# Kernel optimization log

Measured on AMD Instinct MI355X. Metric: run time of the kernel, lower is better.

## Reference

```python
import jax, jax.numpy as jnp
import numpy as np

B, S, V, H, T = 128, 512, 600, 512, 121  # batch, enc steps, vocab, hidden, dec steps (batch_max_length+1)


def setup_inputs() -> dict:
    key = jax.random.key(0)
    ks = jax.random.split(key, 12)
    sc = lambda *shape: 1.0 / np.sqrt(shape[-1])
    inp = {
        "batch_H": jax.random.normal(ks[0], (B, S, V), dtype=jnp.float32),
        "text": jax.random.randint(ks[1], (B, T), 0, V, dtype=jnp.int64),
        # AttentionCell params
        "W_i2h": jax.random.normal(ks[2], (H, V), dtype=jnp.float32) * sc(H, V),
        "W_h2h": jax.random.normal(ks[3], (H, H), dtype=jnp.float32) * sc(H, H),
        "b_h2h": jnp.zeros((H,), dtype=jnp.float32),
        "W_score": jax.random.normal(ks[4], (1, H), dtype=jnp.float32) * sc(1, H),
        # LSTMCell params (torch gate order i, f, g, o); input = context(V) + onehot(V)
        "W_ih": jax.random.normal(ks[5], (4 * H, 2 * V), dtype=jnp.float32) * sc(4 * H, 2 * V),
        "W_hh": jax.random.normal(ks[6], (4 * H, H), dtype=jnp.float32) * sc(4 * H, H),
        "b_ih": jnp.zeros((4 * H,), dtype=jnp.float32),
        "b_hh": jnp.zeros((4 * H,), dtype=jnp.float32),
        # generator
        "W_gen": jax.random.normal(ks[7], (V, H), dtype=jnp.float32) * sc(V, H),
        "b_gen": jnp.zeros((V,), dtype=jnp.float32),
    }
    return inp


def reference(batch_H, text, W_i2h, W_h2h, b_h2h, W_score, W_ih, W_hh, b_ih, b_hh, W_gen, b_gen):
    # Training-path forward: teacher forcing over T = batch_max_length+1 steps.
    # text gets a GO (=0) column prepended; step i consumes text_pad[:, i].
    text_pad = jnp.concatenate([jnp.zeros((B, 1), dtype=text.dtype), text], axis=1)[:, :T]
    onehots = jax.nn.one_hot(text_pad, V, dtype=batch_H.dtype)  # [B, T, V]

    # i2h(batch_H) is constant across timesteps -> hoist out of the loop.
    H_proj = jnp.einsum("bsv,hv->bsh", batch_H, W_i2h)  # [B, S, H]

    def step(carry, onehot_t):
        h, c = carry
        prev_proj = h @ W_h2h.T + b_h2h  # [B, H]
        e = jnp.tanh(H_proj + prev_proj[:, None, :]) @ W_score[0]  # [B, S]
        alpha = jax.nn.softmax(e, axis=1)
        context = jnp.einsum("bs,bsv->bv", alpha, batch_H)  # [B, V]
        x = jnp.concatenate([context, onehot_t], axis=1)  # [B, 2V]
        gates = x @ W_ih.T + b_ih + h @ W_hh.T + b_hh  # [B, 4H]
        i_g, f_g, g_g, o_g = jnp.split(gates, 4, axis=1)
        c_new = jax.nn.sigmoid(f_g) * c + jax.nn.sigmoid(i_g) * jnp.tanh(g_g)
        h_new = jax.nn.sigmoid(o_g) * jnp.tanh(c_new)
        return (h_new, c_new), h_new

    h0 = jnp.zeros((B, H), dtype=batch_H.dtype)
    c0 = jnp.zeros((B, H), dtype=batch_H.dtype)
    _, hiddens = jax.lax.scan(step, (h0, c0), jnp.swapaxes(onehots, 0, 1))  # [T, B, H]
    output_hiddens = jnp.swapaxes(hiddens, 0, 1)  # [B, T, H]
    probs = jax.nn.softmax(output_hiddens @ W_gen.T + b_gen, axis=2)  # [B, T, V]
    return probs
```

## Files before the change

kernel.cpp:

```cpp
#include <hip/hip_runtime.h>
#include <hip/hip_fp16.h>
#include <stdint.h>

#define Bsz 128
#define Ssz 512
#define Vsz 600
#define Hsz 512
#define Tsz 121

__device__ __forceinline__ float fast_tanh(float x) {
  float e = __expf(x + x);
  return 1.0f - __fdividef(2.0f, 1.0f + e);
}

__global__ __launch_bounds__(256) void k_wt(const float* __restrict__ Wi,
                                            float* __restrict__ WiT) {
  __shared__ float T[32][25];
  int k0 = blockIdx.x * 24, c0 = blockIdx.y * 32;
  for (int idx = threadIdx.x; idx < 32 * 24; idx += 256) {
    int i = idx / 24, j = idx - i * 24;
    T[i][j] = Wi[(size_t)(c0 + i) * 600 + k0 + j];
  }
  __syncthreads();
  for (int idx = threadIdx.x; idx < 24 * 32; idx += 256) {
    int j = idx >> 5, i = idx & 31;
    WiT[(size_t)(k0 + j) * 512 + c0 + i] = T[i][j];
  }
}

__global__ __launch_bounds__(256) void k_hp(const float* __restrict__ bH,
                                            const float* __restrict__ WiT,
                                            __half* __restrict__ Hp,
                                            __half* __restrict__ bHT) {
  __shared__ __align__(16) float As[16][604];
  int m0 = blockIdx.x * 16;
  for (int idx = threadIdx.x; idx < 16 * 600; idx += 256) {
    int r = idx / 600, k = idx - r * 600;
    As[r][k] = bH[(size_t)(m0 + r) * 600 + k];
  }
  __syncthreads();
  {
    int b = blockIdx.x >> 5, s0 = (blockIdx.x & 31) * 16;
    for (int v = threadIdx.x; v < 600; v += 256) {
      __half hbuf[16];
#pragma unroll
      for (int r = 0; r < 16; ++r) hbuf[r] = __float2half(As[r][v]);
      float4* dst = (float4*)&bHT[((size_t)b * 600 + v) * 512 + s0];
      dst[0] = ((float4*)hbuf)[0];
      dst[1] = ((float4*)hbuf)[1];
    }
  }
  int rg = threadIdx.x & 3, cg = threadIdx.x >> 2;
  int r0 = rg * 4;
  for (int pass = 0; pass < 2; ++pass) {
    int c0 = pass * 256 + cg * 4;
    float acc[4][4] = {};
    for (int k = 0; k < 600; k += 4) {
      float4 w0 = *(const float4*)&WiT[(size_t)(k + 0) * 512 + c0];
      float4 w1 = *(const float4*)&WiT[(size_t)(k + 1) * 512 + c0];
      float4 w2 = *(const float4*)&WiT[(size_t)(k + 2) * 512 + c0];
      float4 w3 = *(const float4*)&WiT[(size_t)(k + 3) * 512 + c0];
#pragma unroll
      for (int i = 0; i < 4; ++i) {
        float4 a = *(const float4*)&As[r0 + i][k];
        acc[i][0] += a.x * w0.x + a.y * w1.x + a.z * w2.x + a.w * w3.x;
        acc[i][1] += a.x * w0.y + a.y * w1.y + a.z * w2.y + a.w * w3.y;
        acc[i][2] += a.x * w0.z + a.y * w1.z + a.z * w2.z + a.w * w3.z;
        acc[i][3] += a.x * w0.w + a.y * w1.w + a.z * w2.w + a.w * w3.w;
      }
    }
#pragma unroll
    for (int i = 0; i < 4; ++i) {
      __half2 p01 = __floats2half2_rn(acc[i][0], acc[i][1]);
      __half2 p23 = __floats2half2_rn(acc[i][2], acc[i][3]);
      union { __half2 h2[2]; float2 f2; } u;
      u.h2[0] = p01; u.h2[1] = p23;
      *(float2*)&Hp[(size_t)(m0 + r0 + i) * Hsz + c0] = u.f2;
    }
  }
}

__global__ __launch_bounds__(256) void k_pp(const float* __restrict__ hprev,
                                            const float* __restrict__ W,
                                            const float* __restrict__ bias,
                                            float* __restrict__ pp) {
  __shared__ __align__(16) float hs[512];
  __shared__ float part[128];
  int b = blockIdx.x, jq = blockIdx.y;
  int tid = threadIdx.x;
  hs[tid] = hprev[b * Hsz + tid];
  hs[tid + 256] = hprev[b * Hsz + 256 + tid];
  __syncthreads();
  int jl = tid & 127, kh = tid >> 7;
  int j = jq * 128 + jl;
  const float* wrow = W + (size_t)j * Hsz + kh * 256;
  const float* hp = hs + kh * 256;
  float acc = 0.f;
#pragma unroll 4
  for (int k = 0; k < 256; k += 4) {
    float4 w = *(const float4*)(wrow + k);
    float4 h4 = *(const float4*)(hp + k);
    acc += w.x * h4.x + w.y * h4.y + w.z * h4.z + w.w * h4.w;
  }
  if (kh == 1) part[jl] = acc;
  __syncthreads();
  if (kh == 0) pp[b * Hsz + j] = acc + part[jl] + bias[j];
}

__global__ __launch_bounds__(512) void k_e(const __half* __restrict__ Hp,
                                           const float* __restrict__ pp,
                                           const float* __restrict__ Wsc,
                                           float* __restrict__ ev) {
  __shared__ __align__(16) float pps[512];
  __shared__ __align__(16) float wss[512];
  __shared__ float part[4][128];
  int b = blockIdx.x >> 2, tile = blockIdx.x & 3;
  int tid = threadIdx.x;
  pps[tid] = pp[b * Hsz + tid];
  wss[tid] = Wsc[tid];
  __syncthreads();
  int sl = tid & 127, kq = tid >> 7;
  int s = tile * 128 + sl;
  const __half* hrow = Hp + ((size_t)b * Ssz + s) * Hsz + kq * 128;
  const float* pk = pps + kq * 128;
  const float* wk = wss + kq * 128;
  float acc = 0.f;
#pragma unroll 8
  for (int k = 0; k < 128; k += 8) {
    float4 raw = *(const float4*)(hrow + k);
    const __half2* h2p = (const __half2*)&raw;
    float2 f0 = __half22float2(h2p[0]);
    float2 f1 = __half22float2(h2p[1]);
    float2 f2 = __half22float2(h2p[2]);
    float2 f3 = __half22float2(h2p[3]);
    acc += wk[k + 0] * fast_tanh(f0.x + pk[k + 0]);
    acc += wk[k + 1] * fast_tanh(f0.y + pk[k + 1]);
    acc += wk[k + 2] * fast_tanh(f1.x + pk[k + 2]);
    acc += wk[k + 3] * fast_tanh(f1.y + pk[k + 3]);
    acc += wk[k + 4] * fast_tanh(f2.x + pk[k + 4]);
    acc += wk[k + 5] * fast_tanh(f2.y + pk[k + 5]);
    acc += wk[k + 6] * fast_tanh(f3.x + pk[k + 6]);
    acc += wk[k + 7] * fast_tanh(f3.y + pk[k + 7]);
  }
  part[kq][sl] = acc;
  __syncthreads();
  if (kq == 0)
    ev[b * Ssz + s] = (part[0][sl] + part[1][sl]) + (part[2][sl] + part[3][sl]);
}

__global__ __launch_bounds__(256) void k_ctx(const __half* __restrict__ bHT,
                                             const float* __restrict__ ev,
                                             float* __restrict__ ctx) {
  __shared__ __align__(16) float al[512];
  __shared__ float red[8];
  int b = blockIdx.x, vc = blockIdx.y;
  int tid = threadIdx.x, wv = tid >> 6, ln = tid & 63;
  float e0 = ev[b * Ssz + tid], e1 = ev[b * Ssz + 256 + tid];
  float m = fmaxf(e0, e1);
#pragma unroll
  for (int off = 32; off > 0; off >>= 1) m = fmaxf(m, __shfl_xor(m, off));
  if (ln == 0) red[wv] = m;
  __syncthreads();
  m = fmaxf(fmaxf(red[0], red[1]), fmaxf(red[2], red[3]));
  float x0 = __expf(e0 - m), x1 = __expf(e1 - m);
  float sum = x0 + x1;
#pragma unroll
  for (int off = 32; off > 0; off >>= 1) sum += __shfl_xor(sum, off);
  if (ln == 0) red[4 + wv] = sum;
  __syncthreads();
  sum = (red[4] + red[5]) + (red[6] + red[7]);
  float inv = __fdividef(1.f, sum);
  al[tid] = x0 * inv;
  al[tid + 256] = x1 * inv;
  __syncthreads();
  int v = vc * 200 + tid;
  if (tid < 200) {
    const __half* row = bHT + ((size_t)b * Vsz + v) * Ssz;
    float a0 = 0.f, a1 = 0.f, a2 = 0.f, a3 = 0.f;
#pragma unroll 8
    for (int s = 0; s < Ssz; s += 8) {
      float4 raw = *(const float4*)(row + s);
      const __half2* h2p = (const __half2*)&raw;
      float2 f0 = __half22float2(h2p[0]);
      float2 f1 = __half22float2(h2p[1]);
      float2 f2 = __half22float2(h2p[2]);
      float2 f3 = __half22float2(h2p[3]);
      float4 aa = *(const float4*)&al[s];
      float4 ab = *(const float4*)&al[s + 4];
      a0 += aa.x * f0.x + aa.y * f0.y;
      a1 += aa.z * f1.x + aa.w * f1.y;
      a2 += ab.x * f2.x + ab.y * f2.y;
      a3 += ab.z * f3.x + ab.w * f3.y;
    }
    ctx[b * Vsz + v] = (a0 + a1) + (a2 + a3);
  }
}

struct ShG { float xs[8][1112]; float4 part[8][32]; };

__global__ __launch_bounds__(512) void k_gates(
    const float* __restrict__ ctx, const float* __restrict__ hprev,
    const float* __restrict__ Wih, const float* __restrict__ Whh,
    const float* __restrict__ bih, const float* __restrict__ bhh,
    const int* __restrict__ text, int t,
    const float* __restrict__ cin, float* __restrict__ cout,
    float* __restrict__ hnextf, __half* __restrict__ hnext16) {
  __shared__ __align__(16) ShG G;
  const int bid = blockIdx.x, tid = threadIdx.x;
  const int jt = (bid & 7) * 2 + ((bid >> 3) & 1);
  const int bt = bid >> 4;
  int b0 = bt * 8, j0 = jt * 32;
  for (int idx = tid; idx < 8 * 600; idx += 512) {
    int r = idx / 600, k = idx - r * 600;
    G.xs[r][k] = ctx[(b0 + r) * Vsz + k];
  }
  for (int idx = tid; idx < 8 * 512; idx += 512) {
    int r = idx >> 9, k = idx & 511;
    G.xs[r][600 + k] = hprev[(b0 + r) * Hsz + k];
  }
  __syncthreads();
  int bi = tid >> 6, jl = tid & 31, kh = (tid >> 5) & 1;
  int bb = b0 + bi, j = j0 + jl;
  float a0 = 0.f, a1 = 0.f, a2 = 0.f, a3 = 0.f;
  const float* xr = G.xs[bi];
  const float* w0 = Wih + (size_t)(0 * Hsz + j) * 1200 + kh * 300;
  const float* w1 = Wih + (size_t)(1 * Hsz + j) * 1200 + kh * 300;
  const float* w2 = Wih + (size_t)(2 * Hsz + j) * 1200 + kh * 300;
  const float* w3 = Wih + (size_t)(3 * Hsz + j) * 1200 + kh * 300;
  const float* xc = xr + kh * 300;
#pragma unroll 2
  for (int k = 0; k < 300; k += 4) {
    float4 x4 = *(const float4*)(xc + k);
    float4 q0 = *(const float4*)(w0 + k);
    a0 += x4.x * q0.x + x4.y * q0.y + x4.z * q0.z + x4.w * q0.w;
    float4 q1 = *(const float4*)(w1 + k);
    a1 += x4.x * q1.x + x4.y * q1.y + x4.z * q1.z + x4.w * q1.w;
    float4 q2 = *(const float4*)(w2 + k);
    a2 += x4.x * q2.x + x4.y * q2.y + x4.z * q2.z + x4.w * q2.w;
    float4 q3 = *(const float4*)(w3 + k);
    a3 += x4.x * q3.x + x4.y * q3.y + x4.z * q3.z + x4.w * q3.w;
  }
  const float* v0 = Whh + (size_t)(0 * Hsz + j) * Hsz + kh * 256;
  const float* v1 = Whh + (size_t)(1 * Hsz + j) * Hsz + kh * 256;
  const float* v2 = Whh + (size_t)(2 * Hsz + j) * Hsz + kh * 256;
  const float* v3 = Whh + (size_t)(3 * Hsz + j) * Hsz + kh * 256;
  const float* xh = xr + 600 + kh * 256;
#pragma unroll 2
  for (int k = 0; k < 256; k += 4) {
    float4 x4 = *(const float4*)(xh + k);
    float4 q0 = *(const float4*)(v0 + k);
    a0 += x4.x * q0.x + x4.y * q0.y + x4.z * q0.z + x4.w * q0.w;
    float4 q1 = *(const float4*)(v1 + k);
    a1 += x4.x * q1.x + x4.y * q1.y + x4.z * q1.z + x4.w * q1.w;
    float4 q2 = *(const float4*)(v2 + k);
    a2 += x4.x * q2.x + x4.y * q2.y + x4.z * q2.z + x4.w * q2.w;
    float4 q3 = *(const float4*)(v3 + k);
    a3 += x4.x * q3.x + x4.y * q3.y + x4.z * q3.z + x4.w * q3.w;
  }
  if (kh == 1) {
    int tk = (t == 0) ? 0 : text[bb * Tsz + (t - 1)];
    a0 += Wih[(size_t)(0 * Hsz + j) * 1200 + 600 + tk];
    a1 += Wih[(size_t)(1 * Hsz + j) * 1200 + 600 + tk];
    a2 += Wih[(size_t)(2 * Hsz + j) * 1200 + 600 + tk];
    a3 += Wih[(size_t)(3 * Hsz + j) * 1200 + 600 + tk];
    G.part[bi][jl] = make_float4(a0, a1, a2, a3);
  }
  __syncthreads();
  if (kh == 0) {
    float4 p = G.part[bi][jl];
    a0 += p.x + bih[j] + bhh[j];
    a1 += p.y + bih[512 + j] + bhh[512 + j];
    a2 += p.z + bih[1024 + j] + bhh[1024 + j];
    a3 += p.w + bih[1536 + j] + bhh[1536 + j];
    float ig = 1.f / (1.f + __expf(-a0));
    float fg = 1.f / (1.f + __expf(-a1));
    float gg = fast_tanh(a2);
    float og = 1.f / (1.f + __expf(-a3));
    float c = fg * cin[bb * Hsz + j] + ig * gg;
    float hN = og * fast_tanh(c);
    cout[bb * Hsz + j] = c;
    hnextf[bb * Hsz + j] = hN;
    hnext16[(size_t)bb * Hsz + j] = __float2half(hN);
  }
}

__global__ __launch_bounds__(256) void k_gen(const __half* __restrict__ hid16,
                                             const float* __restrict__ Wg,
                                             const float* __restrict__ bg,
                                             float* __restrict__ out) {
  __shared__ __align__(16) float sm[16 * 600];
  int m0 = blockIdx.x * 16;
  for (int idx = threadIdx.x; idx < 16 * 64; idx += 256) {
    int r = idx >> 6, k8 = (idx & 63) * 8;
    int m = m0 + r;
    int bb = m / Tsz, tt = m - bb * Tsz;
    float4 raw = *(const float4*)&hid16[((size_t)tt * Bsz + bb) * Hsz + k8];
    const __half2* h2p = (const __half2*)&raw;
    float2 f0 = __half22float2(h2p[0]);
    float2 f1 = __half22float2(h2p[1]);
    float2 f2 = __half22float2(h2p[2]);
    float2 f3 = __half22float2(h2p[3]);
    float* d = &sm[r * 520 + k8];
    d[0] = f0.x; d[1] = f0.y; d[2] = f1.x; d[3] = f1.y;
    d[4] = f2.x; d[5] = f2.y; d[6] = f3.x; d[7] = f3.y;
  }
  __syncthreads();
  int rg = threadIdx.x & 3, cg = threadIdx.x >> 2;
  int r0 = rg * 4;
  bool has2 = (cg < 22);
  float acc[12][4] = {};
  for (int k = 0; k < 512; k += 4) {
    float4 a[4];
#pragma unroll
    for (int i = 0; i < 4; ++i) a[i] = *(const float4*)&sm[(r0 + i) * 520 + k];
#pragma unroll
    for (int p = 0; p < 3; ++p) {
      if (p == 2 && !has2) continue;
#pragma unroll
      for (int i = 0; i < 4; ++i) {
        int c = p * 256 + cg * 4 + i;
        float4 w = *(const float4*)&Wg[(size_t)c * Hsz + k];
        int ci = p * 4 + i;
#pragma unroll
        for (int r = 0; r < 4; ++r)
          acc[ci][r] += a[r].x * w.x + a[r].y * w.y + a[r].z * w.z + a[r].w * w.w;
      }
    }
  }
  __syncthreads();
#pragma unroll
  for (int p = 0; p < 3; ++p) {
    if (p == 2 && !has2) continue;
#pragma unroll
    for (int i = 0; i < 4; ++i) {
      int c = p * 256 + cg * 4 + i;
      float bgc = bg[c];
#pragma unroll
      for (int r = 0; r < 4; ++r) sm[(r0 + r) * 600 + c] = acc[p * 4 + i][r] + bgc;
    }
  }
  __syncthreads();
  int wv = threadIdx.x >> 6, ln = threadIdx.x & 63;
  for (int r = wv; r < 16; r += 4) {
    float* row = sm + r * 600;
    float mx = -1e30f;
    for (int c = ln; c < 600; c += 64) mx = fmaxf(mx, row[c]);
#pragma unroll
    for (int off = 32; off > 0; off >>= 1) mx = fmaxf(mx, __shfl_xor(mx, off));
    float ssum = 0.f;
    for (int c = ln; c < 600; c += 64) {
      float ex = __expf(row[c] - mx);
      row[c] = ex;
      ssum += ex;
    }
#pragma unroll
    for (int off = 32; off > 0; off >>= 1) ssum += __shfl_xor(ssum, off);
    float inv = __fdividef(1.f, ssum);
    float* op = out + (size_t)(m0 + r) * 600;
    for (int c = ln; c < 600; c += 64) op[c] = row[c] * inv;
  }
}

extern "C" void kernel_launch(void* const* d_in, const int* in_sizes, int n_in,
                              void* d_out, int out_size, void* d_ws, size_t ws_size,
                              hipStream_t stream) {
  const float* bH = (const float*)d_in[0];
  const int* text = (const int*)d_in[1];
  const float* Wi2h = (const float*)d_in[2];
  const float* Wh2h = (const float*)d_in[3];
  const float* bh2h = (const float*)d_in[4];
  const float* Wsc = (const float*)d_in[5];
  const float* Wih = (const float*)d_in[6];
  const float* Whh = (const float*)d_in[7];
  const float* bih = (const float*)d_in[8];
  const float* bhh = (const float*)d_in[9];
  const float* Wg = (const float*)d_in[10];
  const float* bg = (const float*)d_in[11];
  float* out = (float*)d_out;

  char* ws = (char*)d_ws;
  size_t off = 0;
  __half* Hp16 = (__half*)(ws + off);  off += (size_t)Bsz * Ssz * Hsz * 2;
  __half* bHT = (__half*)(ws + off);   off += (size_t)Bsz * Vsz * Ssz * 2;
  __half* hid16 = (__half*)(ws + off); off += (size_t)Tsz * Bsz * Hsz * 2;
  float* WiT = (float*)(ws + off);     off += (size_t)600 * 512 * 4;
  float* h_pp = (float*)(ws + off);    off += (size_t)2 * Bsz * Hsz * 4;
  float* cb = (float*)(ws + off);      off += (size_t)2 * Bsz * Hsz * 4;
  float* pp = (float*)(ws + off);      off += (size_t)Bsz * Hsz * 4;
  float* ev = (float*)(ws + off);      off += (size_t)Bsz * Ssz * 4;
  float* ctx = (float*)(ws + off);     off += (size_t)Bsz * Vsz * 4;

  hipMemsetAsync(h_pp, 0, (size_t)2 * Bsz * Hsz * 4, stream);
  hipMemsetAsync(cb, 0, (size_t)2 * Bsz * Hsz * 4, stream);

  k_wt<<<dim3(25, 16), 256, 0, stream>>>(Wi2h, WiT);
  k_hp<<<(Bsz * Ssz) / 16, 256, 0, stream>>>(bH, WiT, Hp16, bHT);

  for (int t = 0; t < Tsz; ++t) {
    const float* hprev = h_pp + (size_t)(t & 1) * Bsz * Hsz;
    float* hnextf = h_pp + (size_t)((t + 1) & 1) * Bsz * Hsz;
    const float* cin = cb + (size_t)(t & 1) * Bsz * Hsz;
    float* cout = cb + (size_t)((t + 1) & 1) * Bsz * Hsz;
    k_pp<<<dim3(Bsz, 4), 256, 0, stream>>>(hprev, Wh2h, bh2h, pp);
    k_e<<<Bsz * 4, 512, 0, stream>>>(Hp16, pp, Wsc, ev);
    k_ctx<<<dim3(Bsz, 3), 256, 0, stream>>>(bHT, ev, ctx);
    k_gates<<<256, 512, 0, stream>>>(ctx, hprev, Wih, Whh, bih, bhh, text, t,
                                     cin, cout, hnextf,
                                     hid16 + (size_t)t * Bsz * Hsz);
  }

  k_gen<<<(Bsz * Tsz) / 16, 256, 0, stream>>>(hid16, Wg, bg, out);
}
```

Baseline: 27.49 ms.

## Split reductions across more threads and blocks in all per-step recurrent kernels

Each per-timestep kernel gets a finer work split. k_pp reduces over four K-slices, k_e uses 8 tiles of 64 sequence positions with 8-way K-splits, and k_ctx splits the S dimension across 8 wavefronts with 10 V-chunks per batch. k_gates processes 4 batch rows per block with each thread computing two gates, doubling the grid. The goal is more parallelism and memory-level concurrency in these small, latency-bound launches, at the cost of extra shared-memory reductions and redundant softmax recomputation in k_ctx.

```diff
diff --git a/kernel.cpp b/kernel.cpp
--- a/kernel.cpp
+++ b/kernel.cpp
@@ -80,53 +80,53 @@
   }
 }
 
-__global__ __launch_bounds__(256) void k_pp(const float* __restrict__ hprev,
-                                            const float* __restrict__ W,
-                                            const float* __restrict__ bias,
-                                            float* __restrict__ pp) {
+__global__ __launch_bounds__(512, 4) void k_pp(const float* __restrict__ hprev,
+                                               const float* __restrict__ W,
+                                               const float* __restrict__ bias,
+                                               float* __restrict__ pp) {
   __shared__ __align__(16) float hs[512];
-  __shared__ float part[128];
+  __shared__ float part[4][128];
   int b = blockIdx.x, jq = blockIdx.y;
   int tid = threadIdx.x;
   hs[tid] = hprev[b * Hsz + tid];
-  hs[tid + 256] = hprev[b * Hsz + 256 + tid];
-  __syncthreads();
-  int jl = tid & 127, kh = tid >> 7;
+  __syncthreads();
+  int jl = tid & 127, kq = tid >> 7;
   int j = jq * 128 + jl;
-  const float* wrow = W + (size_t)j * Hsz + kh * 256;
-  const float* hp = hs + kh * 256;
+  const float* wrow = W + (size_t)j * Hsz + kq * 128;
+  const float* hp = hs + kq * 128;
   float acc = 0.f;
-#pragma unroll 4
-  for (int k = 0; k < 256; k += 4) {
+#pragma unroll 8
+  for (int k = 0; k < 128; k += 4) {
     float4 w = *(const float4*)(wrow + k);
     float4 h4 = *(const float4*)(hp + k);
     acc += w.x * h4.x + w.y * h4.y + w.z * h4.z + w.w * h4.w;
   }
-  if (kh == 1) part[jl] = acc;
-  __syncthreads();
-  if (kh == 0) pp[b * Hsz + j] = acc + part[jl] + bias[j];
-}
-
-__global__ __launch_bounds__(512) void k_e(const __half* __restrict__ Hp,
-                                           const float* __restrict__ pp,
-                                           const float* __restrict__ Wsc,
-                                           float* __restrict__ ev) {
+  part[kq][jl] = acc;
+  __syncthreads();
+  if (kq == 0)
+    pp[b * Hsz + j] = (part[0][jl] + part[1][jl]) + (part[2][jl] + part[3][jl]) + bias[j];
+}
+
+__global__ __launch_bounds__(512, 8) void k_e(const __half* __restrict__ Hp,
+                                              const float* __restrict__ pp,
+                                              const float* __restrict__ Wsc,
+                                              float* __restrict__ ev) {
   __shared__ __align__(16) float pps[512];
   __shared__ __align__(16) float wss[512];
-  __shared__ float part[4][128];
-  int b = blockIdx.x >> 2, tile = blockIdx.x & 3;
+  __shared__ float part[8][64];
+  int b = blockIdx.x >> 3, tile = blockIdx.x & 7;
   int tid = threadIdx.x;
   pps[tid] = pp[b * Hsz + tid];
   wss[tid] = Wsc[tid];
   __syncthreads();
-  int sl = tid & 127, kq = tid >> 7;
-  int s = tile * 128 + sl;
-  const __half* hrow = Hp + ((size_t)b * Ssz + s) * Hsz + kq * 128;
-  const float* pk = pps + kq * 128;
-  const float* wk = wss + kq * 128;
+  int sl = tid & 63, kq = tid >> 6;
+  int s = tile * 64 + sl;
+  const __half* hrow = Hp + ((size_t)b * Ssz + s) * Hsz + kq * 64;
+  const float* pk = pps + kq * 64;
+  const float* wk = wss + kq * 64;
   float acc = 0.f;
-#pragma unroll 8
-  for (int k = 0; k < 128; k += 8) {
+#pragma unroll
+  for (int k = 0; k < 64; k += 8) {
     float4 raw = *(const float4*)(hrow + k);
     const __half2* h2p = (const __half2*)&raw;
     float2 f0 = __half22float2(h2p[0]);
@@ -144,61 +144,73 @@
   }
   part[kq][sl] = acc;
   __syncthreads();
-  if (kq == 0)
-    ev[b * Ssz + s] = (part[0][sl] + part[1][sl]) + (part[2][sl] + part[3][sl]);
-}
-
-__global__ __launch_bounds__(256) void k_ctx(const __half* __restrict__ bHT,
-                                             const float* __restrict__ ev,
-                                             float* __restrict__ ctx) {
+  if (kq == 0) {
+    float r = ((part[0][sl] + part[1][sl]) + (part[2][sl] + part[3][sl])) +
+              ((part[4][sl] + part[5][sl]) + (part[6][sl] + part[7][sl]));
+    ev[b * Ssz + s] = r;
+  }
+}
+
+__global__ __launch_bounds__(512, 8) void k_ctx(const __half* __restrict__ bHT,
+                                                const float* __restrict__ ev,
+                                                float* __restrict__ ctx) {
   __shared__ __align__(16) float al[512];
-  __shared__ float red[8];
-  int b = blockIdx.x, vc = blockIdx.y;
+  __shared__ float red[16];
+  __shared__ float part[8][64];
+  int b = blockIdx.x, vq = blockIdx.y;
   int tid = threadIdx.x, wv = tid >> 6, ln = tid & 63;
-  float e0 = ev[b * Ssz + tid], e1 = ev[b * Ssz + 256 + tid];
-  float m = fmaxf(e0, e1);
+  float e = ev[b * Ssz + tid];
+  float m = e;
 #pragma unroll
   for (int off = 32; off > 0; off >>= 1) m = fmaxf(m, __shfl_xor(m, off));
   if (ln == 0) red[wv] = m;
   __syncthreads();
-  m = fmaxf(fmaxf(red[0], red[1]), fmaxf(red[2], red[3]));
-  float x0 = __expf(e0 - m), x1 = __expf(e1 - m);
-  float sum = x0 + x1;
+  m = fmaxf(fmaxf(fmaxf(red[0], red[1]), fmaxf(red[2], red[3])),
+            fmaxf(fmaxf(red[4], red[5]), fmaxf(red[6], red[7])));
+  float x = __expf(e - m);
+  float sum = x;
 #pragma unroll
   for (int off = 32; off > 0; off >>= 1) sum += __shfl_xor(sum, off);
-  if (ln == 0) red[4 + wv] = sum;
-  __syncthreads();
-  sum = (red[4] + red[5]) + (red[6] + red[7]);
-  float inv = __fdividef(1.f, sum);
-  al[tid] = x0 * inv;
-  al[tid + 256] = x1 * inv;
-  __syncthreads();
-  int v = vc * 200 + tid;
-  if (tid < 200) {
-    const __half* row = bHT + ((size_t)b * Vsz + v) * Ssz;
-    float a0 = 0.f, a1 = 0.f, a2 = 0.f, a3 = 0.f;
-#pragma unroll 8
-    for (int s = 0; s < Ssz; s += 8) {
-      float4 raw = *(const float4*)(row + s);
-      const __half2* h2p = (const __half2*)&raw;
-      float2 f0 = __half22float2(h2p[0]);
-      float2 f1 = __half22float2(h2p[1]);
-      float2 f2 = __half22float2(h2p[2]);
-      float2 f3 = __half22float2(h2p[3]);
-      float4 aa = *(const float4*)&al[s];
-      float4 ab = *(const float4*)&al[s + 4];
-      a0 += aa.x * f0.x + aa.y * f0.y;
-      a1 += aa.z * f1.x + aa.w * f1.y;
-      a2 += ab.x * f2.x + ab.y * f2.y;
-      a3 += ab.z * f3.x + ab.w * f3.y;
-    }
-    ctx[b * Vsz + v] = (a0 + a1) + (a2 + a3);
-  }
-}
-
-struct ShG { float xs[8][1112]; float4 part[8][32]; };
-
-__global__ __launch_bounds__(512) void k_gates(
+  if (ln == 0) red[8 + wv] = sum;
+  __syncthreads();
+  sum = ((red[8] + red[9]) + (red[10] + red[11])) +
+        ((red[12] + red[13]) + (red[14] + red[15]));
+  al[tid] = x * __fdividef(1.f, sum);
+  __syncthreads();
+
+  int sg = wv, vl = ln;
+  int v = vq * 60 + vl;
+  int vv = v < 600 ? v : 599;
+  const __half* row = bHT + ((size_t)b * Vsz + vv) * Ssz + sg * 64;
+  const float* ap = al + sg * 64;
+  float a0 = 0.f, a1 = 0.f, a2 = 0.f, a3 = 0.f;
+#pragma unroll
+  for (int s2 = 0; s2 < 64; s2 += 8) {
+    float4 raw = *(const float4*)(row + s2);
+    const __half2* h2p = (const __half2*)&raw;
+    float2 f0 = __half22float2(h2p[0]);
+    float2 f1 = __half22float2(h2p[1]);
+    float2 f2 = __half22float2(h2p[2]);
+    float2 f3 = __half22float2(h2p[3]);
+    float4 aa = *(const float4*)&ap[s2];
+    float4 ab = *(const float4*)&ap[s2 + 4];
+    a0 += aa.x * f0.x + aa.y * f0.y;
+    a1 += aa.z * f1.x + aa.w * f1.y;
+    a2 += ab.x * f2.x + ab.y * f2.y;
+    a3 += ab.z * f3.x + ab.w * f3.y;
+  }
+  part[sg][vl] = (a0 + a1) + (a2 + a3);
+  __syncthreads();
+  if (sg == 0 && vl < 60) {
+    float r = ((part[0][vl] + part[1][vl]) + (part[2][vl] + part[3][vl])) +
+              ((part[4][vl] + part[5][vl]) + (part[6][vl] + part[7][vl]));
+    ctx[b * Vsz + v] = r;
+  }
+}
+
+struct ShG { float xs[4][1112]; float2 part[4][32][4]; };
+
+__global__ __launch_bounds__(512, 2) void k_gates(
     const float* __restrict__ ctx, const float* __restrict__ hprev,
     const float* __restrict__ Wih, const float* __restrict__ Whh,
     const float* __restrict__ bih, const float* __restrict__ bhh,
@@ -207,75 +219,66 @@
     float* __restrict__ hnextf, __half* __restrict__ hnext16) {
   __shared__ __align__(16) ShG G;
   const int bid = blockIdx.x, tid = threadIdx.x;
-  const int jt = (bid & 7) * 2 + ((bid >> 3) & 1);
+  const int jt = ((bid & 7) << 1) | ((bid >> 3) & 1);
   const int bt = bid >> 4;
-  int b0 = bt * 8, j0 = jt * 32;
-  for (int idx = tid; idx < 8 * 600; idx += 512) {
+  int b0 = bt * 4, j0 = jt * 32;
+  for (int idx = tid; idx < 4 * 600; idx += 512) {
     int r = idx / 600, k = idx - r * 600;
     G.xs[r][k] = ctx[(b0 + r) * Vsz + k];
   }
-  for (int idx = tid; idx < 8 * 512; idx += 512) {
+  for (int idx = tid; idx < 4 * 512; idx += 512) {
     int r = idx >> 9, k = idx & 511;
     G.xs[r][600 + k] = hprev[(b0 + r) * Hsz + k];
   }
   __syncthreads();
-  int bi = tid >> 6, jl = tid & 31, kh = (tid >> 5) & 1;
+  int bi = tid >> 7, r = tid & 127;
+  int jl = r >> 2, kh = (r >> 1) & 1, gh = r & 1;
   int bb = b0 + bi, j = j0 + jl;
-  float a0 = 0.f, a1 = 0.f, a2 = 0.f, a3 = 0.f;
+  int ga = gh * 2, gb = gh * 2 + 1;
+  float accA = 0.f, accB = 0.f;
   const float* xr = G.xs[bi];
-  const float* w0 = Wih + (size_t)(0 * Hsz + j) * 1200 + kh * 300;
-  const float* w1 = Wih + (size_t)(1 * Hsz + j) * 1200 + kh * 300;
-  const float* w2 = Wih + (size_t)(2 * Hsz + j) * 1200 + kh * 300;
-  const float* w3 = Wih + (size_t)(3 * Hsz + j) * 1200 + kh * 300;
+  const float* wa = Wih + (size_t)(ga * Hsz + j) * 1200 + kh * 300;
+  const float* wb = Wih + (size_t)(gb * Hsz + j) * 1200 + kh * 300;
   const float* xc = xr + kh * 300;
-#pragma unroll 2
+#pragma unroll 4
   for (int k = 0; k < 300; k += 4) {
     float4 x4 = *(const float4*)(xc + k);
-    float4 q0 = *(const float4*)(w0 + k);
-    a0 += x4.x * q0.x + x4.y * q0.y + x4.z * q0.z + x4.w * q0.w;
-    float4 q1 = *(const float4*)(w1 + k);
-    a1 += x4.x * q1.x + x4.y * q1.y + x4.z * q1.z + x4.w * q1.w;
-    float4 q2 = *(const float4*)(w2 + k);
-    a2 += x4.x * q2.x + x4.y * q2.y + x4.z * q2.z + x4.w * q2.w;
-    float4 q3 = *(const float4*)(w3 + k);
-    a3 += x4.x * q3.x + x4.y * q3.y + x4.z * q3.z + x4.w * q3.w;
-  }
-  const float* v0 = Whh + (size_t)(0 * Hsz + j) * Hsz + kh * 256;
-  const float* v1 = Whh + (size_t)(1 * Hsz + j) * Hsz + kh * 256;
-  const float* v2 = Whh + (size_t)(2 * Hsz + j) * Hsz + kh * 256;
-  const float* v3 = Whh + (size_t)(3 * Hsz + j) * Hsz + kh * 256;
+    float4 qa = *(const float4*)(wa + k);
+    accA += x4.x * qa.x + x4.y * qa.y + x4.z * qa.z + x4.w * qa.w;
+    float4 qb = *(const float4*)(wb + k);
+    accB += x4.x * qb.x + x4.y * qb.y + x4.z * qb.z + x4.w * qb.w;
+  }
+  const float* va = Whh + (size_t)(ga * Hsz + j) * Hsz + kh * 256;
+  const float* vb = Whh + (size_t)(gb * Hsz + j) * Hsz + kh * 256;
   const float* xh = xr + 600 + kh * 256;
-#pragma unroll 2
+#pragma unroll 4
   for (int k = 0; k < 256; k += 4) {
     float4 x4 = *(const float4*)(xh + k);
-    float4 q0 = *(const float4*)(v0 + k);
-    a0 += x4.x * q0.x + x4.y * q0.y + x4.z * q0.z + x4.w * q0.w;
-    float4 q1 = *(const float4*)(v1 + k);
-    a1 += x4.x * q1.x + x4.y * q1.y + x4.z * q1.z + x4.w * q1.w;
-    float4 q2 = *(const float4*)(v2 + k);
-    a2 += x4.x * q2.x + x4.y * q2.y + x4.z * q2.z + x4.w * q2.w;
-    float4 q3 = *(const float4*)(v3 + k);
-    a3 += x4.x * q3.x + x4.y * q3.y + x4.z * q3.z + x4.w * q3.w;
+    float4 qa = *(const float4*)(va + k);
+    accA += x4.x * qa.x + x4.y * qa.y + x4.z * qa.z + x4.w * qa.w;
+    float4 qb = *(const float4*)(vb + k);
+    accB += x4.x * qb.x + x4.y * qb.y + x4.z * qb.z + x4.w * qb.w;
   }
   if (kh == 1) {
     int tk = (t == 0) ? 0 : text[bb * Tsz + (t - 1)];
-    a0 += Wih[(size_t)(0 * Hsz + j) * 1200 + 600 + tk];
-    a1 += Wih[(size_t)(1 * Hsz + j) * 1200 + 600 + tk];
-    a2 += Wih[(size_t)(2 * Hsz + j) * 1200 + 600 + tk];
-    a3 += Wih[(size_t)(3 * Hsz + j) * 1200 + 600 + tk];
-    G.part[bi][jl] = make_float4(a0, a1, a2, a3);
-  }
-  __syncthreads();
-  if (kh == 0) {
-    float4 p = G.part[bi][jl];
-    a0 += p.x + bih[j] + bhh[j];
-    a1 += p.y + bih[512 + j] + bhh[512 + j];
-    a2 += p.z + bih[1024 + j] + bhh[1024 + j];
-    a3 += p.w + bih[1536 + j] + bhh[1536 + j];
-    float ig = 1.f / (1.f + __expf(-a0));
-    float fg = 1.f / (1.f + __expf(-a1));
-    float gg = fast_tanh(a2);
-    float og = 1.f / (1.f + __expf(-a3));
+    accA += Wih[(size_t)(ga * Hsz + j) * 1200 + 600 + tk];
+    accB += Wih[(size_t)(gb * Hsz + j) * 1200 + 600 + tk];
+  }
+  G.part[bi][jl][kh * 2 + gh] = make_float2(accA, accB);
+  __syncthreads();
+  if (kh == 0 && gh == 0) {
+    float2 p00 = G.part[bi][jl][0];
+    float2 p01 = G.part[bi][jl][1];
+    float2 p10 = G.part[bi][jl][2];
+    float2 p11 = G.part[bi][jl][3];
+    float g0 = p00.x + p10.x + bih[j] + bhh[j];
+    float g1 = p00.y + p10.y + bih[512 + j] + bhh[512 + j];
+    float g2 = p01.x + p11.x + bih[1024 + j] + bhh[1024 + j];
+    float g3 = p01.y + p11.y + bih[1536 + j] + bhh[1536 + j];
+    float ig = 1.f / (1.f + __expf(-g0));
+    float fg = 1.f / (1.f + __expf(-g1));
+    float gg = fast_tanh(g2);
+    float og = 1.f / (1.f + __expf(-g3));
     float c = fg * cin[bb * Hsz + j] + ig * gg;
     float hN = og * fast_tanh(c);
     cout[bb * Hsz + j] = c;
@@ -401,10 +404,10 @@
     float* hnextf = h_pp + (size_t)((t + 1) & 1) * Bsz * Hsz;
     const float* cin = cb + (size_t)(t & 1) * Bsz * Hsz;
     float* cout = cb + (size_t)((t + 1) & 1) * Bsz * Hsz;
-    k_pp<<<dim3(Bsz, 4), 256, 0, stream>>>(hprev, Wh2h, bh2h, pp);
-    k_e<<<Bsz * 4, 512, 0, stream>>>(Hp16, pp, Wsc, ev);
-    k_ctx<<<dim3(Bsz, 3), 256, 0, stream>>>(bHT, ev, ctx);
-    k_gates<<<256, 512, 0, stream>>>(ctx, hprev, Wih, Whh, bih, bhh, text, t,
+    k_pp<<<dim3(Bsz, 4), 512, 0, stream>>>(hprev, Wh2h, bh2h, pp);
+    k_e<<<Bsz * 8, 512, 0, stream>>>(Hp16, pp, Wsc, ev);
+    k_ctx<<<dim3(Bsz, 10), 512, 0, stream>>>(bHT, ev, ctx);
+    k_gates<<<512, 512, 0, stream>>>(ctx, hprev, Wih, Whh, bih, bhh, text, t,
                                      cin, cout, hnextf,
                                      hid16 + (size_t)t * Bsz * Hsz);
   }
```

Result: faster. 24.51 ms (-10.8%).
